# Kernel optimization log

Hardware: AMD Instinct MI355X
Metric: run time of the kernel (lower is better)

## Reference

```python
import jax, jax.numpy as jnp
import numpy as np

B, S, E, H = 4, 2048, 1024, 16
DH = E // H  # head_dim = 64


def setup_inputs() -> dict:
    key = jax.random.key(0)
    k1, k2, k3 = jax.random.split(key, 3)
    x = jax.random.normal(k1, (B, S, E), dtype=jnp.float32)
    # xavier-uniform-like scale for dense kernels
    Wqkv = jax.random.normal(k2, (E, 3 * E), dtype=jnp.float32) * (1.0 / np.sqrt(E))
    Wout = jax.random.normal(k3, (E, E), dtype=jnp.float32) * (1.0 / np.sqrt(E))
    return {"x": x, "Wqkv": Wqkv, "Wout": Wout}


def reference(x, Wqkv, Wout):
    b, s, e = x.shape
    qkv = jnp.einsum("bse,ef->bsf", x, Wqkv)            # [B,S,3E]
    qkv = qkv.reshape(b, s, H, 3 * DH).transpose(0, 2, 1, 3)  # [B,H,S,3*DH]
    q, k, v = jnp.split(qkv, 3, axis=-1)                # each [B,H,S,DH]
    scale = 1.0 / jnp.sqrt(jnp.asarray(DH, dtype=x.dtype))
    scores = jnp.einsum("bhqd,bhkd->bhqk", q, k) * scale  # [B,H,S,S] materialized
    attn = jax.nn.softmax(scores, axis=-1)
    values = jnp.einsum("bhqk,bhkd->bhqd", attn, v)     # [B,H,S,DH]
    values = values.transpose(0, 2, 1, 3).reshape(b, s, e)
    out = jnp.einsum("bse,ef->bsf", values, Wout)       # [B,S,E]
    return out
```

## Files before the change

kernel.cpp:

```cpp
#include <hip/hip_runtime.h>

typedef __attribute__((ext_vector_type(8))) __bf16 bf16x8;
typedef __attribute__((ext_vector_type(4))) float f32x4;

#define LOG2E 1.4426950408889634f
#define QSCALE (0.125f * LOG2E)

static __device__ __forceinline__ void gl_lds16(const void* g, void* l) {
  __builtin_amdgcn_global_load_lds(
      (__attribute__((address_space(1))) void*)(g),
      (__attribute__((address_space(3))) void*)(l), 16, 0, 0);
}

__global__ __launch_bounds__(256) void convert_f32_bf16(const float* __restrict__ in,
                                                        __bf16* __restrict__ out,
                                                        int n8) {
  const int i = blockIdx.x * 256 + threadIdx.x;
  if (i >= n8) return;
  const f32x4 a = *(const f32x4*)(in + (size_t)i * 8);
  const f32x4 b = *(const f32x4*)(in + (size_t)i * 8 + 4);
  bf16x8 o;
#pragma unroll
  for (int j = 0; j < 4; ++j) o[j] = (__bf16)a[j];
#pragma unroll
  for (int j = 0; j < 4; ++j) o[4 + j] = (__bf16)b[j];
  *(bf16x8*)(out + (size_t)i * 8) = o;
}

__global__ __launch_bounds__(256) void transpose_f32_bf16(
    const float* __restrict__ in, __bf16* __restrict__ out, int R, int C) {
  __shared__ __bf16 tile[64][72];
  const int t = threadIdx.x;
  const int c0 = blockIdx.x * 64;
  const int r0 = blockIdx.y * 64;
  const int lr = t >> 2;
  const int lc = (t & 3) * 16;
  const float* src = in + (size_t)(r0 + lr) * C + c0 + lc;
  bf16x8 w0, w1;
#pragma unroll
  for (int j = 0; j < 2; ++j) {
    const f32x4 a = *(const f32x4*)(src + j * 8);
    const f32x4 b = *(const f32x4*)(src + j * 8 + 4);
    bf16x8 o;
#pragma unroll
    for (int k = 0; k < 4; ++k) o[k] = (__bf16)a[k];
#pragma unroll
    for (int k = 0; k < 4; ++k) o[4 + k] = (__bf16)b[k];
    *(bf16x8*)&tile[lr][lc + j * 8] = o;
  }
  __syncthreads();
#pragma unroll
  for (int j = 0; j < 8; ++j) {
    w0[j] = tile[lc + j][lr];
    w1[j] = tile[lc + 8 + j][lr];
  }
  __bf16* dst = out + (size_t)(c0 + lr) * R + r0 + lc;
  *(bf16x8*)dst = w0;
  *(bf16x8*)(dst + 8) = w1;
}


#define STAGE_A(TT, KH)                                                  \
  do {                                                                   \
    const int kg_ = (TT) * 64 + (KH) * 32;                               \
    char* d_ = lds + ((TT) & 1) * 32768 + (KH) * 16384 + t * 16;         \
    gl_lds16(Ab + g0 + kg_, d_);                                         \
    gl_lds16(Ab + g1 + kg_, d_ + 8192);                                  \
  } while (0)

#define STAGE_B(TT, KH)                                                  \
  do {                                                                   \
    const int kg_ = (TT) * 64 + (KH) * 32;                               \
    char* d_ = lds + 65536 + ((TT) & 1) * 32768 + (KH) * 16384 + t * 16; \
    gl_lds16(Bb + g0 + kg_, d_);                                         \
    gl_lds16(Bb + g1 + kg_, d_ + 8192);                                  \
  } while (0)

#define READ_A(MIH, KK)                                                          \
  do {                                                                           \
    const char* p_ = lds + buf * 32768 + (KK) * 16384 +                          \
                     (wm * 8 + (MIH) * 4) * 1024 + lfo;                          \
    a0 = *(const bf16x8*)p_;                                                     \
    a1 = *(const bf16x8*)(p_ + 1024);                                            \
    a2 = *(const bf16x8*)(p_ + 2048);                                            \
    a3 = *(const bf16x8*)(p_ + 3072);                                            \
  } while (0)

#define READ_B(KK)                                                               \
  do {                                                                           \
    const char* p_ = lds + 65536 + buf * 32768 + (KK) * 16384 + wn * 4096 + lfo; \
    b0 = *(const bf16x8*)p_;                                                     \
    b1 = *(const bf16x8*)(p_ + 1024);                                            \
    b2 = *(const bf16x8*)(p_ + 2048);                                            \
    b3 = *(const bf16x8*)(p_ + 3072);                                            \
  } while (0)

#define MROW(H, MI, AV)                                                          \
  acc[(H) * 4 + (MI)][0] =                                                       \
      __builtin_amdgcn_mfma_f32_16x16x32_bf16(AV, b0, acc[(H) * 4 + (MI)][0], 0, 0, 0); \
  acc[(H) * 4 + (MI)][1] =                                                       \
      __builtin_amdgcn_mfma_f32_16x16x32_bf16(AV, b1, acc[(H) * 4 + (MI)][1], 0, 0, 0); \
  acc[(H) * 4 + (MI)][2] =                                                       \
      __builtin_amdgcn_mfma_f32_16x16x32_bf16(AV, b2, acc[(H) * 4 + (MI)][2], 0, 0, 0); \
  acc[(H) * 4 + (MI)][3] =                                                       \
      __builtin_amdgcn_mfma_f32_16x16x32_bf16(AV, b3, acc[(H) * 4 + (MI)][3], 0, 0, 0);

#define MFMA16(H)                      \
  do {                                 \
    __builtin_amdgcn_s_setprio(1);     \
    MROW(H, 0, a0)                     \
    MROW(H, 1, a1)                     \
    MROW(H, 2, a2)                     \
    MROW(H, 3, a3)                     \
    __builtin_amdgcn_s_setprio(0);     \
  } while (0)

template <int EPI>
__global__ __launch_bounds__(512, 2) void gemm256(
    const __bf16* __restrict__ A, const __bf16* __restrict__ Bt,
    float* __restrict__ Cf, __bf16* __restrict__ q_ws, __bf16* __restrict__ k_ws,
    __bf16* __restrict__ vT_ws, int M, int N, int K) {
  (void)M;
  extern __shared__ char lds[];
  const int t = threadIdx.x;
  const int lane = t & 63;
  const int quad = lane >> 4, l15 = lane & 15;
  const int w = t >> 6;
  const int wm = w >> 2, wn = w & 3;

  const int gx = gridDim.x;
  int lid = blockIdx.y * gx + blockIdx.x;
  lid = (lid & 7) * ((gx * gridDim.y) >> 3) + (lid >> 3);
  const int m0 = (lid % gx) * 256;
  const int n0 = (lid / gx) * 256;

  int rowS[2], kcS[2];
#pragma unroll
  for (int l = 0; l < 2; ++l) {
    const int LB = l * 8192 + t * 16;
    const int r_in = (LB >> 6) & 15;
    const int ch = ((LB >> 5) & 1) ^ ((r_in >> 3) & 1);
    rowS[l] = (LB >> 10) * 16 + r_in;
    kcS[l] = ch * 16 + ((LB >> 4) & 1) * 8;
  }
  const __bf16* Ab = A + (size_t)m0 * K;
  const __bf16* Bb = Bt + (size_t)n0 * K;
  const size_t g0 = (size_t)rowS[0] * K + kcS[0];
  const size_t g1 = (size_t)rowS[1] * K + kcS[1];

  const int lfo = l15 * 64 + ((((quad >> 1) ^ (l15 >> 3)) & 1) << 5) + ((quad & 1) << 4);

  const f32x4 fzero = {0.f, 0.f, 0.f, 0.f};
  f32x4 acc[8][4];
#pragma unroll
  for (int i = 0; i < 8; ++i)
#pragma unroll
    for (int j = 0; j < 4; ++j) acc[i][j] = fzero;

  const int nt = K >> 6;
  bf16x8 a0, a1, a2, a3, b0, b1, b2, b3;

  STAGE_A(0, 0);
  STAGE_B(0, 0);
  STAGE_A(0, 1);
  STAGE_B(0, 1);
  if (nt > 1) {
    STAGE_A(1, 0);
    STAGE_B(1, 0);
    asm volatile("s_waitcnt vmcnt(4)");
  } else {
    asm volatile("s_waitcnt vmcnt(0)");
  }
  __builtin_amdgcn_s_barrier();

  for (int tt = 0; tt < nt; ++tt) {
    const int buf = tt & 1;
    READ_A(0, 0);
    READ_B(0);
    if (tt + 1 < nt) STAGE_A(tt + 1, 1);
    __builtin_amdgcn_s_barrier();
    asm volatile("s_waitcnt lgkmcnt(0)");
    MFMA16(0);
    __builtin_amdgcn_s_barrier();
    READ_A(1, 0);
    if (tt + 1 < nt) STAGE_B(tt + 1, 1);
    __builtin_amdgcn_s_barrier();
    asm volatile("s_waitcnt lgkmcnt(0)");
    MFMA16(1);
    __builtin_amdgcn_s_barrier();
    READ_A(0, 1);
    READ_B(1);
    if (tt + 2 < nt) STAGE_A(tt + 2, 0);
    __builtin_amdgcn_s_barrier();
    asm volatile("s_waitcnt lgkmcnt(0)");
    MFMA16(0);
    __builtin_amdgcn_s_barrier();
    READ_A(1, 1);
    if (tt + 2 < nt) STAGE_B(tt + 2, 0);
    __builtin_amdgcn_s_barrier();
    asm volatile("s_waitcnt lgkmcnt(0)");
    MFMA16(1);
    if (tt + 2 < nt)
      asm volatile("s_waitcnt vmcnt(4)");
    else
      asm volatile("s_waitcnt vmcnt(0)");
    __builtin_amdgcn_s_barrier();
  }

#pragma unroll
  for (int mi = 0; mi < 8; ++mi) {
#pragma unroll
    for (int r = 0; r < 4; ++r) {
      const int row = m0 + wm * 128 + mi * 16 + quad * 4 + r;
#pragma unroll
      for (int ni = 0; ni < 4; ++ni) {
        const int col = n0 + wn * 64 + ni * 16 + l15;
        const float v = acc[mi][ni][r];
        if (EPI == 0) {
          const int b = row >> 11, s = row & 2047;
          const int h = col / 192;
          const int rr = col - h * 192;
          const int ty = rr >> 6, d = rr & 63;
          const int bh = b * 16 + h;
          if (ty == 0)
            q_ws[((size_t)bh * 2048 + s) * 64 + d] = (__bf16)(v * QSCALE);
          else if (ty == 1)
            k_ws[((size_t)bh * 2048 + s) * 64 + d] = (__bf16)v;
          else
            vT_ws[((size_t)bh * 64 + d) * 2048 + s] = (__bf16)v;
        } else {
          Cf[(size_t)row * N + col] = v;
        }
      }
    }
  }
}

__global__ __launch_bounds__(256) void flash_attn(
    const __bf16* __restrict__ q_ws, const __bf16* __restrict__ k_ws,
    const __bf16* __restrict__ vT_ws, __bf16* __restrict__ values, int bh0) {
  __shared__ __bf16 sK[64][72];
  __shared__ __bf16 sVt[64][72];
  __shared__ __bf16 sP[4][32][72];
  const int t = threadIdx.x;
  const int lane = t & 63, w = t >> 6, quad = lane >> 4, l15 = lane & 15;
  const int qt = blockIdx.x;
  const int bh = blockIdx.y + bh0;
  const __bf16* Qb = q_ws + (size_t)bh * 2048 * 64;
  const __bf16* Kb = k_ws + (size_t)bh * 2048 * 64;
  const __bf16* Vtb = vT_ws + (size_t)bh * 64 * 2048;
  const int qrow0 = qt * 128 + w * 32;

  bf16x8 qf[2][2];
#pragma unroll
  for (int mi = 0; mi < 2; ++mi)
#pragma unroll
    for (int ks = 0; ks < 2; ++ks)
      qf[mi][ks] = *(const bf16x8*)(Qb + (size_t)(qrow0 + mi * 16 + l15) * 64 +
                                    ks * 32 + quad * 8);

  bf16x8 ones;
#pragma unroll
  for (int j = 0; j < 8; ++j) ones[j] = (__bf16)1.0f;

  const f32x4 fzero = {0.f, 0.f, 0.f, 0.f};
  f32x4 accO[2][4];
  f32x4 accL[2];
#pragma unroll
  for (int mi = 0; mi < 2; ++mi) {
    accL[mi] = fzero;
#pragma unroll
    for (int ni = 0; ni < 4; ++ni) accO[mi][ni] = fzero;
  }

  const int srow = t >> 2;
  const int scol = (t & 3) * 16;

  bf16x8 ka, kb2, va, vb;
  {
    const __bf16* ks0 = Kb + (size_t)srow * 64 + scol;
    ka = *(const bf16x8*)ks0;
    kb2 = *(const bf16x8*)(ks0 + 8);
    const __bf16* vs0 = Vtb + (size_t)srow * 2048 + scol;
    va = *(const bf16x8*)vs0;
    vb = *(const bf16x8*)(vs0 + 8);
  }

  for (int kt = 0; kt < 32; ++kt) {
    *(bf16x8*)&sK[srow][scol] = ka;
    *(bf16x8*)&sK[srow][scol + 8] = kb2;
    *(bf16x8*)&sVt[srow][scol] = va;
    *(bf16x8*)&sVt[srow][scol + 8] = vb;
    __syncthreads();

    if (kt < 31) {
      const __bf16* ksn = Kb + (size_t)((kt + 1) * 64 + srow) * 64 + scol;
      ka = *(const bf16x8*)ksn;
      kb2 = *(const bf16x8*)(ksn + 8);
      const __bf16* vsn = Vtb + (size_t)srow * 2048 + (kt + 1) * 64 + scol;
      va = *(const bf16x8*)vsn;
      vb = *(const bf16x8*)(vsn + 8);
    }

    f32x4 accS[2][4];
#pragma unroll
    for (int mi = 0; mi < 2; ++mi)
#pragma unroll
      for (int ni = 0; ni < 4; ++ni) accS[mi][ni] = fzero;
#pragma unroll
    for (int ks = 0; ks < 2; ++ks) {
      bf16x8 kf[4];
#pragma unroll
      for (int ni = 0; ni < 4; ++ni)
        kf[ni] = *(const bf16x8*)&sK[ni * 16 + l15][ks * 32 + quad * 8];
#pragma unroll
      for (int mi = 0; mi < 2; ++mi)
#pragma unroll
        for (int ni = 0; ni < 4; ++ni)
          accS[mi][ni] = __builtin_amdgcn_mfma_f32_16x16x32_bf16(
              qf[mi][ks], kf[ni], accS[mi][ni], 0, 0, 0);
    }

#pragma unroll
    for (int mi = 0; mi < 2; ++mi) {
#pragma unroll
      for (int r = 0; r < 4; ++r) {
        const int prow = mi * 16 + quad * 4 + r;
#pragma unroll
        for (int ni = 0; ni < 4; ++ni) {
          const float p = __builtin_amdgcn_exp2f(accS[mi][ni][r]);
          sP[w][prow][ni * 16 + l15] = (__bf16)p;
        }
      }
    }
    __threadfence_block();

#pragma unroll
    for (int ks = 0; ks < 2; ++ks) {
      bf16x8 vf[4], pf[2];
#pragma unroll
      for (int ni = 0; ni < 4; ++ni)
        vf[ni] = *(const bf16x8*)&sVt[ni * 16 + l15][ks * 32 + quad * 8];
#pragma unroll
      for (int mi = 0; mi < 2; ++mi)
        pf[mi] = *(const bf16x8*)&sP[w][mi * 16 + l15][ks * 32 + quad * 8];
#pragma unroll
      for (int mi = 0; mi < 2; ++mi) {
#pragma unroll
        for (int ni = 0; ni < 4; ++ni)
          accO[mi][ni] = __builtin_amdgcn_mfma_f32_16x16x32_bf16(
              pf[mi], vf[ni], accO[mi][ni], 0, 0, 0);
        accL[mi] = __builtin_amdgcn_mfma_f32_16x16x32_bf16(pf[mi], ones, accL[mi],
                                                           0, 0, 0);
      }
    }
    __syncthreads();
  }

  const int b = bh >> 4, h = bh & 15;
#pragma unroll
  for (int mi = 0; mi < 2; ++mi) {
#pragma unroll
    for (int r = 0; r < 4; ++r) {
      const float inv = 1.0f / accL[mi][r];
      const int s = qrow0 + mi * 16 + quad * 4 + r;
#pragma unroll
      for (int ni = 0; ni < 4; ++ni)
        values[((size_t)(b * 2048 + s)) * 1024 + h * 64 + ni * 16 + l15] =
            (__bf16)(accO[mi][ni][r] * inv);
    }
  }
}

extern "C" void kernel_launch(void* const* d_in, const int* in_sizes, int n_in,
                              void* d_out, int out_size, void* d_ws, size_t ws_size,
                              hipStream_t stream) {
  (void)out_size; (void)ws_size;
  float* out = (float*)d_out;
  char* wsb = (char*)d_ws;
  __bf16* xb = (__bf16*)(wsb + 256);
  __bf16* WqkvT = xb + 8388608;
  __bf16* WoutT = WqkvT + 3145728;
  __bf16* q_ws = WoutT + 1048576;
  __bf16* k_ws = q_ws + 8388608;
  __bf16* vT_ws = k_ws + 8388608;
  __bf16* values = xb;

  const float *px = (const float*)d_in[0], *pw = (const float*)d_in[1],
              *po = (const float*)d_in[2];
  for (int i = 0; i < n_in; ++i) {
    if (in_sizes[i] == 8388608) px = (const float*)d_in[i];
    else if (in_sizes[i] == 3145728) pw = (const float*)d_in[i];
    else if (in_sizes[i] == 1048576) po = (const float*)d_in[i];
  }

  hipFuncSetAttribute(reinterpret_cast<const void*>(&gemm256<0>),
                      hipFuncAttributeMaxDynamicSharedMemorySize, 131072);
  hipFuncSetAttribute(reinterpret_cast<const void*>(&gemm256<1>),
                      hipFuncAttributeMaxDynamicSharedMemorySize, 131072);

  convert_f32_bf16<<<4096, 256, 0, stream>>>(px, xb, 1048576);
  transpose_f32_bf16<<<dim3(48, 16), 256, 0, stream>>>(pw, WqkvT, 1024, 3072);
  transpose_f32_bf16<<<dim3(16, 16), 256, 0, stream>>>(po, WoutT, 1024, 1024);
  gemm256<0><<<dim3(32, 12), 512, 131072, stream>>>(xb, WqkvT, nullptr, q_ws, k_ws,
                                                    vT_ws, 8192, 3072, 1024);
  flash_attn<<<dim3(16, 32), 256, 0, stream>>>(q_ws, k_ws, vT_ws, values, 0);
  flash_attn<<<dim3(16, 32), 256, 0, stream>>>(q_ws, k_ws, vT_ws, values, 32);
  gemm256<1><<<dim3(32, 4), 512, 131072, stream>>>(values, WoutT, out, nullptr,
                                                   nullptr, nullptr, 8192, 1024, 1024);
}
```

Baseline: 326.6 us.

## Shrink GEMM tile to 256x128, simplify pipeline, merge flash-attention launches

Changes the GEMM block tile from 256x256 to 256x128. Each wave now computes 8x2 MFMA tiles, and the B operand takes half the LDS, so dynamic LDS drops to 96KB. The K loop is reorganised into two half-steps per iteration with fused A/B reads and fewer barriers, and the XCD-aware block remap is replaced by an explicit mapping. The grid doubles, which gives more blocks for load balancing across CUs at the cost of more A reloads. The two flash-attention launches are also merged into a single 64-wide grid to remove one launch.

```diff
diff --git a/kernel.cpp b/kernel.cpp
--- a/kernel.cpp
+++ b/kernel.cpp
@@ -71,47 +71,41 @@
 #define STAGE_B(TT, KH)                                                  \
   do {                                                                   \
     const int kg_ = (TT) * 64 + (KH) * 32;                               \
-    char* d_ = lds + 65536 + ((TT) & 1) * 32768 + (KH) * 16384 + t * 16; \
+    char* d_ = lds + 65536 + ((TT) & 1) * 16384 + (KH) * 8192 + t * 16;  \
     gl_lds16(Bb + g0 + kg_, d_);                                         \
-    gl_lds16(Bb + g1 + kg_, d_ + 8192);                                  \
   } while (0)
 
-#define READ_A(MIH, KK)                                                          \
+#define READ_AB(KK)                                                              \
   do {                                                                           \
-    const char* p_ = lds + buf * 32768 + (KK) * 16384 +                          \
-                     (wm * 8 + (MIH) * 4) * 1024 + lfo;                          \
-    a0 = *(const bf16x8*)p_;                                                     \
-    a1 = *(const bf16x8*)(p_ + 1024);                                            \
-    a2 = *(const bf16x8*)(p_ + 2048);                                            \
-    a3 = *(const bf16x8*)(p_ + 3072);                                            \
+    const char* pa_ = lds + buf * 32768 + (KK) * 16384 + wm * 8192 + lfo;        \
+    a0 = *(const bf16x8*)pa_;                                                    \
+    a1 = *(const bf16x8*)(pa_ + 1024);                                           \
+    a2 = *(const bf16x8*)(pa_ + 2048);                                           \
+    a3 = *(const bf16x8*)(pa_ + 3072);                                           \
+    a4 = *(const bf16x8*)(pa_ + 4096);                                           \
+    a5 = *(const bf16x8*)(pa_ + 5120);                                           \
+    a6 = *(const bf16x8*)(pa_ + 6144);                                           \
+    a7 = *(const bf16x8*)(pa_ + 7168);                                           \
+    const char* pb_ = lds + 65536 + buf * 16384 + (KK) * 8192 + wn * 2048 + lfo; \
+    b0 = *(const bf16x8*)pb_;                                                    \
+    b1 = *(const bf16x8*)(pb_ + 1024);                                           \
   } while (0)
 
-#define READ_B(KK)                                                               \
-  do {                                                                           \
-    const char* p_ = lds + 65536 + buf * 32768 + (KK) * 16384 + wn * 4096 + lfo; \
-    b0 = *(const bf16x8*)p_;                                                     \
-    b1 = *(const bf16x8*)(p_ + 1024);                                            \
-    b2 = *(const bf16x8*)(p_ + 2048);                                            \
-    b3 = *(const bf16x8*)(p_ + 3072);                                            \
-  } while (0)
-
-#define MROW(H, MI, AV)                                                          \
-  acc[(H) * 4 + (MI)][0] =                                                       \
-      __builtin_amdgcn_mfma_f32_16x16x32_bf16(AV, b0, acc[(H) * 4 + (MI)][0], 0, 0, 0); \
-  acc[(H) * 4 + (MI)][1] =                                                       \
-      __builtin_amdgcn_mfma_f32_16x16x32_bf16(AV, b1, acc[(H) * 4 + (MI)][1], 0, 0, 0); \
-  acc[(H) * 4 + (MI)][2] =                                                       \
-      __builtin_amdgcn_mfma_f32_16x16x32_bf16(AV, b2, acc[(H) * 4 + (MI)][2], 0, 0, 0); \
-  acc[(H) * 4 + (MI)][3] =                                                       \
-      __builtin_amdgcn_mfma_f32_16x16x32_bf16(AV, b3, acc[(H) * 4 + (MI)][3], 0, 0, 0);
-
-#define MFMA16(H)                      \
+#define MROW(MI, AV)                                                             \
+  acc[MI][0] = __builtin_amdgcn_mfma_f32_16x16x32_bf16(AV, b0, acc[MI][0], 0, 0, 0); \
+  acc[MI][1] = __builtin_amdgcn_mfma_f32_16x16x32_bf16(AV, b1, acc[MI][1], 0, 0, 0);
+
+#define MFMA16()                       \
   do {                                 \
     __builtin_amdgcn_s_setprio(1);     \
-    MROW(H, 0, a0)                     \
-    MROW(H, 1, a1)                     \
-    MROW(H, 2, a2)                     \
-    MROW(H, 3, a3)                     \
+    MROW(0, a0)                        \
+    MROW(1, a1)                        \
+    MROW(2, a2)                        \
+    MROW(3, a3)                        \
+    MROW(4, a4)                        \
+    MROW(5, a5)                        \
+    MROW(6, a6)                        \
+    MROW(7, a7)                        \
     __builtin_amdgcn_s_setprio(0);     \
   } while (0)
 
@@ -128,11 +122,10 @@
   const int w = t >> 6;
   const int wm = w >> 2, wn = w & 3;
 
-  const int gx = gridDim.x;
-  int lid = blockIdx.y * gx + blockIdx.x;
-  lid = (lid & 7) * ((gx * gridDim.y) >> 3) + (lid >> 3);
-  const int m0 = (lid % gx) * 256;
-  const int n0 = (lid / gx) * 256;
+  const int olid = blockIdx.y * gridDim.x + blockIdx.x;
+  const int xcd = olid & 7, loc = olid >> 3;
+  const int m0 = (xcd * 4 + (loc & 3)) * 256;
+  const int n0 = (loc >> 2) * 128;
 
   int rowS[2], kcS[2];
 #pragma unroll
@@ -151,14 +144,15 @@
   const int lfo = l15 * 64 + ((((quad >> 1) ^ (l15 >> 3)) & 1) << 5) + ((quad & 1) << 4);
 
   const f32x4 fzero = {0.f, 0.f, 0.f, 0.f};
-  f32x4 acc[8][4];
-#pragma unroll
-  for (int i = 0; i < 8; ++i)
-#pragma unroll
-    for (int j = 0; j < 4; ++j) acc[i][j] = fzero;
+  f32x4 acc[8][2];
+#pragma unroll
+  for (int i = 0; i < 8; ++i) {
+    acc[i][0] = fzero;
+    acc[i][1] = fzero;
+  }
 
   const int nt = K >> 6;
-  bf16x8 a0, a1, a2, a3, b0, b1, b2, b3;
+  bf16x8 a0, a1, a2, a3, a4, a5, a6, a7, b0, b1;
 
   STAGE_A(0, 0);
   STAGE_B(0, 0);
@@ -167,7 +161,7 @@
   if (nt > 1) {
     STAGE_A(1, 0);
     STAGE_B(1, 0);
-    asm volatile("s_waitcnt vmcnt(4)");
+    asm volatile("s_waitcnt vmcnt(3)");
   } else {
     asm volatile("s_waitcnt vmcnt(0)");
   }
@@ -175,36 +169,34 @@
 
   for (int tt = 0; tt < nt; ++tt) {
     const int buf = tt & 1;
-    READ_A(0, 0);
-    READ_B(0);
-    if (tt + 1 < nt) STAGE_A(tt + 1, 1);
+    READ_AB(0);
+    if (tt + 1 < nt) {
+      STAGE_A(tt + 1, 1);
+      STAGE_B(tt + 1, 1);
+    }
     __builtin_amdgcn_s_barrier();
     asm volatile("s_waitcnt lgkmcnt(0)");
-    MFMA16(0);
-    __builtin_amdgcn_s_barrier();
-    READ_A(1, 0);
-    if (tt + 1 < nt) STAGE_B(tt + 1, 1);
-    __builtin_amdgcn_s_barrier();
-    asm volatile("s_waitcnt lgkmcnt(0)");
-    MFMA16(1);
-    __builtin_amdgcn_s_barrier();
-    READ_A(0, 1);
-    READ_B(1);
-    if (tt + 2 < nt) STAGE_A(tt + 2, 0);
-    __builtin_amdgcn_s_barrier();
-    asm volatile("s_waitcnt lgkmcnt(0)");
-    MFMA16(0);
-    __builtin_amdgcn_s_barrier();
-    READ_A(1, 1);
-    if (tt + 2 < nt) STAGE_B(tt + 2, 0);
-    __builtin_amdgcn_s_barrier();
-    asm volatile("s_waitcnt lgkmcnt(0)");
-    MFMA16(1);
-    if (tt + 2 < nt)
-      asm volatile("s_waitcnt vmcnt(4)");
+    MFMA16();
+    if (tt + 1 < nt)
+      asm volatile("s_waitcnt vmcnt(6)");
     else
       asm volatile("s_waitcnt vmcnt(0)");
     __builtin_amdgcn_s_barrier();
+    READ_AB(1);
+    if (tt + 2 < nt) {
+      STAGE_A(tt + 2, 0);
+      STAGE_B(tt + 2, 0);
+    }
+    __builtin_amdgcn_s_barrier();
+    asm volatile("s_waitcnt lgkmcnt(0)");
+    MFMA16();
+    if (tt + 2 < nt)
+      asm volatile("s_waitcnt vmcnt(6)");
+    else if (tt + 1 < nt)
+      asm volatile("s_waitcnt vmcnt(3)");
+    else
+      asm volatile("s_waitcnt vmcnt(0)");
+    __builtin_amdgcn_s_barrier();
   }
 
 #pragma unroll
@@ -213,8 +205,8 @@
     for (int r = 0; r < 4; ++r) {
       const int row = m0 + wm * 128 + mi * 16 + quad * 4 + r;
 #pragma unroll
-      for (int ni = 0; ni < 4; ++ni) {
-        const int col = n0 + wn * 64 + ni * 16 + l15;
+      for (int ni = 0; ni < 2; ++ni) {
+        const int col = n0 + wn * 32 + ni * 16 + l15;
         const float v = acc[mi][ni][r];
         if (EPI == 0) {
           const int b = row >> 11, s = row & 2047;
@@ -395,17 +387,16 @@
   }
 
   hipFuncSetAttribute(reinterpret_cast<const void*>(&gemm256<0>),
-                      hipFuncAttributeMaxDynamicSharedMemorySize, 131072);
+                      hipFuncAttributeMaxDynamicSharedMemorySize, 98304);
   hipFuncSetAttribute(reinterpret_cast<const void*>(&gemm256<1>),
-                      hipFuncAttributeMaxDynamicSharedMemorySize, 131072);
+                      hipFuncAttributeMaxDynamicSharedMemorySize, 98304);
 
   convert_f32_bf16<<<4096, 256, 0, stream>>>(px, xb, 1048576);
   transpose_f32_bf16<<<dim3(48, 16), 256, 0, stream>>>(pw, WqkvT, 1024, 3072);
   transpose_f32_bf16<<<dim3(16, 16), 256, 0, stream>>>(po, WoutT, 1024, 1024);
-  gemm256<0><<<dim3(32, 12), 512, 131072, stream>>>(xb, WqkvT, nullptr, q_ws, k_ws,
-                                                    vT_ws, 8192, 3072, 1024);
-  flash_attn<<<dim3(16, 32), 256, 0, stream>>>(q_ws, k_ws, vT_ws, values, 0);
-  flash_attn<<<dim3(16, 32), 256, 0, stream>>>(q_ws, k_ws, vT_ws, values, 32);
-  gemm256<1><<<dim3(32, 4), 512, 131072, stream>>>(values, WoutT, out, nullptr,
-                                                   nullptr, nullptr, 8192, 1024, 1024);
-}
+  gemm256<0><<<dim3(32, 24), 512, 98304, stream>>>(xb, WqkvT, nullptr, q_ws, k_ws,
+                                                   vT_ws, 8192, 3072, 1024);
+  flash_attn<<<dim3(16, 64), 256, 0, stream>>>(q_ws, k_ws, vT_ws, values, 0);
+  gemm256<1><<<dim3(32, 8), 512, 98304, stream>>>(values, WoutT, out, nullptr,
+                                                  nullptr, nullptr, 8192, 1024, 1024);
+}
```

Measured after the change: 310.0 us. 5.1% less time.
